# Performance work log

Hardware: AMD Instinct MI355X
Metric: run time of the kernel (lower is better)

The kernel has to match this reference:

```python
import jax, jax.numpy as jnp
import numpy as np

N_NODES = 100000
N_FEAT = 128
HID = 8
HEADS1 = 8
OUT2 = 32
NEG_SLOPE = 0.2


def gat_conv(x, W, a_src, a_dst, b, src, dst, n_nodes, concat):
    # x: [N, Fin], W: [Fin, H*C], a_src/a_dst: [H, C], b: [H*C] or [C]
    H, C = a_src.shape
    h = (x @ W).reshape(n_nodes, H, C)                      # [N, H, C]
    e_src = jnp.sum(h * a_src, axis=-1)                     # [N, H]
    e_dst = jnp.sum(h * a_dst, axis=-1)                     # [N, H]
    e = jax.nn.leaky_relu(e_src[src] + e_dst[dst], NEG_SLOPE)  # [E, H]
    m = jax.ops.segment_max(e, dst, num_segments=n_nodes)   # [N, H] (self-loops => no empty segment)
    ex = jnp.exp(e - m[dst])                                # [E, H]
    denom = jax.ops.segment_sum(ex, dst, num_segments=n_nodes)
    alpha = ex / denom[dst]                                 # [E, H]
    out = jax.ops.segment_sum(alpha[:, :, None] * h[src], dst, num_segments=n_nodes)  # [N, H, C]
    out = out.reshape(n_nodes, H * C) if concat else out.mean(axis=1)
    return out + b


def setup_inputs() -> dict:
    key = jax.random.key(0)
    ks = jax.random.split(key, 12)
    x = jax.random.normal(ks[0], (N_NODES, N_FEAT), dtype=jnp.float32)
    edge_index = jax.random.randint(ks[1], (2, 3200000), 0, N_NODES, dtype=jnp.int64)
    s1 = 1.0 / np.sqrt(N_FEAT)
    s2 = 1.0 / np.sqrt(HID * HEADS1)
    return {
        "x": x,
        "edge_index": edge_index,
        "W1": jax.random.normal(ks[2], (N_FEAT, HEADS1 * HID), dtype=jnp.float32) * s1,
        "a_src1": jax.random.normal(ks[3], (HEADS1, HID), dtype=jnp.float32) * s2,
        "a_dst1": jax.random.normal(ks[4], (HEADS1, HID), dtype=jnp.float32) * s2,
        "b1": jnp.zeros((HEADS1 * HID,), dtype=jnp.float32),
        "W2": jax.random.normal(ks[5], (HEADS1 * HID, OUT2), dtype=jnp.float32) * s2,
        "a_src2": jax.random.normal(ks[6], (1, OUT2), dtype=jnp.float32) * (1.0 / np.sqrt(OUT2)),
        "a_dst2": jax.random.normal(ks[7], (1, OUT2), dtype=jnp.float32) * (1.0 / np.sqrt(OUT2)),
        "b2": jnp.zeros((OUT2,), dtype=jnp.float32),
        "Wr": jax.random.normal(ks[8], (OUT2, 1), dtype=jnp.float32) * (1.0 / np.sqrt(OUT2)),
        "br": jnp.zeros((1,), dtype=jnp.float32),
    }


def reference(x, edge_index, W1, a_src1, a_dst1, b1, W2, a_src2, a_dst2, b2, Wr, br):
    n = x.shape[0]
    # PyG GATConv default add_self_loops=True
    loops = jnp.arange(n, dtype=edge_index.dtype)
    src = jnp.concatenate([edge_index[0], loops])
    dst = jnp.concatenate([edge_index[1], loops])
    h = gat_conv(x, W1, a_src1, a_dst1, b1, src, dst, n, concat=True)   # [N, 64]
    h = jax.nn.elu(h)
    h = gat_conv(h, W2, a_src2, a_dst2, b2, src, dst, n, concat=False)  # [N, 32]
    pooled = jnp.sum(h, axis=0, keepdims=True)                          # SumAggregation -> [1, 32]
    return pooled @ Wr + br                                             # [1, 1]
```

## Files before the change

### kernel.cpp

```cpp
#include <hip/hip_runtime.h>
#include <math.h>

#define NEG_SLOPE 0.2f
#define FIN 128
#define H1 8
#define F1 64
#define F2 32

#define SHIFT 6
#define BW 64
#define CAP 4096
#define NBMAX 2048

typedef unsigned short ushort_t;
typedef unsigned int uint_t;

static __device__ __forceinline__ ushort_t f2bf(float f) {
    uint_t u = __float_as_uint(f);
    u = (u + 0x7FFFu + ((u >> 16) & 1u)) >> 16;
    return (ushort_t)u;
}
static __device__ __forceinline__ float bf2f(ushort_t h) {
    return __uint_as_float(((uint_t)h) << 16);
}
static __device__ __forceinline__ uint_t packAB(float e) {
    return (uint_t)f2bf(__expf(e)) | ((uint_t)f2bf(__expf(NEG_SLOPE * e)) << 16);
}

__global__ void gemm1_kernel(const float* __restrict__ x, const float* __restrict__ W1,
                             const float* __restrict__ a_src, const float* __restrict__ a_dst,
                             ushort_t* __restrict__ h1, uint_t* __restrict__ sp,
                             float* __restrict__ ed, int N) {
    __shared__ float xs[16][FIN];
    int tid = threadIdx.x;
    int n0 = blockIdx.x * 16;
    for (int i = tid; i < 16 * FIN; i += 256) {
        int nn = n0 + (i >> 7);
        xs[i >> 7][i & 127] = (nn < N) ? x[(size_t)nn * FIN + (i & 127)] : 0.f;
    }
    __syncthreads();
    int wv = tid >> 6, j = tid & 63;
    int nb = wv << 2;
    float a0 = 0.f, a1 = 0.f, a2 = 0.f, a3 = 0.f;
#pragma unroll 2
    for (int k = 0; k < FIN; k += 4) {
        float w0 = W1[(k + 0) * F1 + j];
        float w1 = W1[(k + 1) * F1 + j];
        float w2 = W1[(k + 2) * F1 + j];
        float w3 = W1[(k + 3) * F1 + j];
        float4 x0 = *(const float4*)&xs[nb + 0][k];
        float4 x1 = *(const float4*)&xs[nb + 1][k];
        float4 x2 = *(const float4*)&xs[nb + 2][k];
        float4 x3 = *(const float4*)&xs[nb + 3][k];
        a0 = fmaf(x0.x, w0, fmaf(x0.y, w1, fmaf(x0.z, w2, fmaf(x0.w, w3, a0))));
        a1 = fmaf(x1.x, w0, fmaf(x1.y, w1, fmaf(x1.z, w2, fmaf(x1.w, w3, a1))));
        a2 = fmaf(x2.x, w0, fmaf(x2.y, w1, fmaf(x2.z, w2, fmaf(x2.w, w3, a2))));
        a3 = fmaf(x3.x, w0, fmaf(x3.y, w1, fmaf(x3.z, w2, fmaf(x3.w, w3, a3))));
    }
    float as = a_src[j], ad = a_dst[j];
    float av[4] = {a0, a1, a2, a3};
#pragma unroll
    for (int t = 0; t < 4; ++t) {
        int n = n0 + nb + t;
        if (n >= N) break;
        h1[(size_t)n * F1 + j] = f2bf(av[t]);
        float vs = av[t] * as;
        float vd = av[t] * ad;
#pragma unroll
        for (int off = 4; off >= 1; off >>= 1) {
            vs += __shfl_down(vs, off, 8);
            vd += __shfl_down(vd, off, 8);
        }
        if ((j & 7) == 0) {
            sp[n * H1 + (j >> 3)] = packAB(vs);
            ed[n * H1 + (j >> 3)] = vd;
        }
    }
}

__global__ void zerob_kernel(int* __restrict__ bcnt, int NB, float* __restrict__ pooled) {
    int t = blockIdx.x * blockDim.x + threadIdx.x;
    int stride = gridDim.x * blockDim.x;
    for (int i = t; i < NB; i += stride) bcnt[i] = 0;
    if (t == 0) pooled[0] = 0.f;
}

__global__ void bhist_kernel(const int* __restrict__ ei, int E, int N,
                             int* __restrict__ bcnt, int NB) {
    __shared__ int h[NBMAX];
    int tid = threadIdx.x;
    for (int i = tid; i < NB; i += 256) h[i] = 0;
    __syncthreads();
    int EN = E + N;
    int chunk = (EN + gridDim.x - 1) / gridDim.x;
    int e0 = blockIdx.x * chunk;
    int e1 = e0 + chunk; if (e1 > EN) e1 = EN;
    for (int t = e0 + tid; t < e1; t += 256) {
        int d = (t < E) ? ei[E + t] : (t - E);
        atomicAdd(&h[d >> SHIFT], 1);
    }
    __syncthreads();
    for (int i = tid; i < NB; i += 256)
        if (h[i]) atomicAdd(&bcnt[i], h[i]);
}

__global__ void bscan_kernel(const int* __restrict__ bcnt, int NB,
                             int* __restrict__ boff, int* __restrict__ bcur) {
    int lane = threadIdx.x;
    int chunk = (NB + 63) >> 6;
    int lo = lane * chunk;
    int hi = lo + chunk; if (hi > NB) hi = NB;
    int sum = 0;
    for (int i = lo; i < hi; ++i) sum += bcnt[i];
    int e = sum;
#pragma unroll
    for (int o = 1; o < 64; o <<= 1) {
        int v = __shfl_up(e, o, 64);
        if (lane >= o) e += v;
    }
    e -= sum;
    int run = e;
    for (int i = lo; i < hi; ++i) {
        int c = bcnt[i];
        boff[i] = run;
        bcur[i] = run;
        run += c;
    }
}

__global__ void bscat_kernel(const int* __restrict__ ei, int E, int N,
                             int* __restrict__ bcur, uint_t* __restrict__ pk, int NB) {
    __shared__ int lh[NBMAX];
    __shared__ int lc[NBMAX];
    int tid = threadIdx.x;
    for (int i = tid; i < NB; i += 256) lh[i] = 0;
    __syncthreads();
    int EN = E + N;
    int chunk = (EN + gridDim.x - 1) / gridDim.x;
    int e0 = blockIdx.x * chunk;
    int e1 = e0 + chunk; if (e1 > EN) e1 = EN;
    for (int t = e0 + tid; t < e1; t += 256) {
        int d = (t < E) ? ei[E + t] : (t - E);
        atomicAdd(&lh[d >> SHIFT], 1);
    }
    __syncthreads();
    for (int i = tid; i < NB; i += 256) {
        int c = lh[i];
        lc[i] = c ? atomicAdd(&bcur[i], c) : 0;
    }
    __syncthreads();
    for (int t = e0 + tid; t < e1; t += 256) {
        int s, d;
        if (t < E) { s = ei[t]; d = ei[E + t]; } else { s = d = t - E; }
        int pos = atomicAdd(&lc[d >> SHIFT], 1);
        pk[pos] = ((uint_t)s << SHIFT) | (uint_t)(d & (BW - 1));
    }
}

__global__ void edge1_gather(const int* __restrict__ bcnt, const int* __restrict__ boff,
                             const uint_t* __restrict__ pk,
                             const uint_t* __restrict__ sp, const float* __restrict__ ed,
                             const ushort_t* __restrict__ h1, float* __restrict__ o1, int N) {
    int b = blockIdx.x;
    int d0 = b << SHIFT;
    int cnt = bcnt[b];
    int gbase = boff[b];
    int tid = threadIdx.x;
    int wv = tid >> 6;
    int L = tid & 63;
    int q = L >> 4;
    int c4 = (L & 15) << 2;
    int hL = (L & 15) >> 1;
    __shared__ int ldeg[BW];
    __shared__ int loff[BW];
    __shared__ int lcur[BW];
    __shared__ int lsrc[CAP];
    if (cnt <= CAP) {
        if (tid < BW) ldeg[tid] = 0;
        __syncthreads();
        for (int k = tid; k < cnt; k += 256) atomicAdd(&ldeg[pk[gbase + k] & (BW - 1)], 1);
        __syncthreads();
        if (tid < 64) {
            int v = ldeg[tid];
            int e = v;
#pragma unroll
            for (int o = 1; o < 64; o <<= 1) {
                int u = __shfl_up(e, o, 64);
                if (tid >= o) e += u;
            }
            e -= v;
            loff[tid] = e;
            lcur[tid] = e;
        }
        __syncthreads();
        for (int k = tid; k < cnt; k += 256) {
            uint_t v = pk[gbase + k];
            int pos = atomicAdd(&lcur[v & (BW - 1)], 1);
            lsrc[pos] = (int)(v >> SHIFT);
        }
        __syncthreads();
        for (int ld = wv * 16; ld < wv * 16 + 16; ++ld) {
            int d = d0 + ld;
            if (d >= N) break;
            int st = loff[ld], en = st + ldeg[ld];
            float edv = ed[d * H1 + hL];
            float Ad = __expf(edv), Bd = __expf(NEG_SLOPE * edv);
            float ax = 0.f, ay = 0.f, az = 0.f, aw = 0.f, wsum = 0.f;
            for (int k = st; k < en; k += 8) {
                int i0 = k + q, i1 = k + 4 + q;
                bool ok0 = i0 < en, ok1 = i1 < en;
                int s0 = lsrc[ok0 ? i0 : st];
                int s1 = lsrc[ok1 ? i1 : st];
                uint_t u0 = sp[(uint_t)s0 * H1 + hL];
                uint_t u1 = sp[(uint_t)s1 * H1 + hL];
                uint2 hv0 = *(const uint2*)(h1 + ((uint_t)s0 << 6) + c4);
                uint2 hv1 = *(const uint2*)(h1 + ((uint_t)s1 << 6) + c4);
                float w0 = ok0 ? fmaxf(__uint_as_float(u0 << 16) * Ad,
                                       __uint_as_float(u0 & 0xffff0000u) * Bd) : 0.f;
                float w1 = ok1 ? fmaxf(__uint_as_float(u1 << 16) * Ad,
                                       __uint_as_float(u1 & 0xffff0000u) * Bd) : 0.f;
                ax = fmaf(w0, __uint_as_float(hv0.x << 16), ax);
                ay = fmaf(w0, __uint_as_float(hv0.x & 0xffff0000u), ay);
                az = fmaf(w0, __uint_as_float(hv0.y << 16), az);
                aw = fmaf(w0, __uint_as_float(hv0.y & 0xffff0000u), aw);
                ax = fmaf(w1, __uint_as_float(hv1.x << 16), ax);
                ay = fmaf(w1, __uint_as_float(hv1.x & 0xffff0000u), ay);
                az = fmaf(w1, __uint_as_float(hv1.y << 16), az);
                aw = fmaf(w1, __uint_as_float(hv1.y & 0xffff0000u), aw);
                wsum += w0 + w1;
            }
            ax += __shfl_xor(ax, 16, 64); ax += __shfl_xor(ax, 32, 64);
            ay += __shfl_xor(ay, 16, 64); ay += __shfl_xor(ay, 32, 64);
            az += __shfl_xor(az, 16, 64); az += __shfl_xor(az, 32, 64);
            aw += __shfl_xor(aw, 16, 64); aw += __shfl_xor(aw, 32, 64);
            wsum += __shfl_xor(wsum, 16, 64); wsum += __shfl_xor(wsum, 32, 64);
            if (q == 0) {
                float inv = 1.f / wsum;
                float4 r; r.x = ax * inv; r.y = ay * inv; r.z = az * inv; r.w = aw * inv;
                *(float4*)(o1 + (size_t)d * F1 + c4) = r;
            }
        }
    } else {
        for (int ld = wv * 16; ld < wv * 16 + 16; ++ld) {
            int d = d0 + ld;
            if (d >= N) break;
            float edv = ed[d * H1 + hL];
            float Ad = __expf(edv), Bd = __expf(NEG_SLOPE * edv);
            float ax = 0.f, ay = 0.f, az = 0.f, aw = 0.f, wsum = 0.f;
            for (int k0 = 0; k0 < cnt; k0 += 4) {
                int idx = k0 + q;
                bool ok = idx < cnt;
                uint_t v = pk[gbase + (ok ? idx : 0)];
                int s = (int)(v >> SHIFT);
                bool m = ok && ((int)(v & (BW - 1)) == ld);
                uint_t u = sp[(uint_t)s * H1 + hL];
                float w = m ? fmaxf(__uint_as_float(u << 16) * Ad,
                                    __uint_as_float(u & 0xffff0000u) * Bd) : 0.f;
                uint2 hv = *(const uint2*)(h1 + ((uint_t)s << 6) + c4);
                ax = fmaf(w, __uint_as_float(hv.x << 16), ax);
                ay = fmaf(w, __uint_as_float(hv.x & 0xffff0000u), ay);
                az = fmaf(w, __uint_as_float(hv.y << 16), az);
                aw = fmaf(w, __uint_as_float(hv.y & 0xffff0000u), aw);
                wsum += w;
            }
            ax += __shfl_xor(ax, 16, 64); ax += __shfl_xor(ax, 32, 64);
            ay += __shfl_xor(ay, 16, 64); ay += __shfl_xor(ay, 32, 64);
            az += __shfl_xor(az, 16, 64); az += __shfl_xor(az, 32, 64);
            aw += __shfl_xor(aw, 16, 64); aw += __shfl_xor(aw, 32, 64);
            wsum += __shfl_xor(wsum, 16, 64); wsum += __shfl_xor(wsum, 32, 64);
            if (q == 0) {
                float inv = 1.f / wsum;
                float4 r; r.x = ax * inv; r.y = ay * inv; r.z = az * inv; r.w = aw * inv;
                *(float4*)(o1 + (size_t)d * F1 + c4) = r;
            }
        }
    }
}

__global__ void gemm2_kernel(const float* __restrict__ o1, const float* __restrict__ b1,
                             const float* __restrict__ W2,
                             const float* __restrict__ a_src2, const float* __restrict__ a_dst2,
                             ushort_t* __restrict__ h2, uint_t* __restrict__ sp2,
                             float* __restrict__ ed2, int N) {
    int half = threadIdx.x >> 5;
    int n = blockIdx.x * 8 + half;
    int j = threadIdx.x & 31;
    __shared__ float a1s[8][F1];
    if (n < N) {
#pragma unroll
        for (int r = 0; r < 2; ++r) {
            int k = r * 32 + j;
            float v = o1[(size_t)n * F1 + k] + b1[k];
            a1s[half][k] = v > 0.f ? v : expm1f(v);
        }
    }
    __syncthreads();
    if (n >= N) return;
    float acc = 0.f;
#pragma unroll
    for (int k = 0; k < F1; ++k) acc = fmaf(a1s[half][k], W2[k * F2 + j], acc);
    h2[(size_t)n * F2 + j] = f2bf(acc);
    float vs = acc * a_src2[j];
    float vd = acc * a_dst2[j];
#pragma unroll
    for (int off = 16; off >= 1; off >>= 1) {
        vs += __shfl_down(vs, off, 32);
        vd += __shfl_down(vd, off, 32);
    }
    if (j == 0) {
        sp2[n] = packAB(vs);
        ed2[n] = vd;
    }
}

__global__ void edge2_gather(const int* __restrict__ bcnt, const int* __restrict__ boff,
                             const uint_t* __restrict__ pk,
                             const uint_t* __restrict__ sp2, const float* __restrict__ ed2,
                             const ushort_t* __restrict__ h2,
                             const float* __restrict__ b2, const float* __restrict__ Wr,
                             float* __restrict__ pooled, int N) {
    int b = blockIdx.x;
    int d0 = b << SHIFT;
    int cnt = bcnt[b];
    int gbase = boff[b];
    int tid = threadIdx.x;
    int hw = tid >> 5;
    int j = tid & 31;
    __shared__ int ldeg[BW];
    __shared__ int loff[BW];
    __shared__ int lcur[BW];
    __shared__ int lsrc[CAP];
    float wr = Wr[j];
    float b2w = b2[j] * wr;
    float part = 0.f;
    if (cnt <= CAP) {
        if (tid < BW) ldeg[tid] = 0;
        __syncthreads();
        for (int k = tid; k < cnt; k += 256) atomicAdd(&ldeg[pk[gbase + k] & (BW - 1)], 1);
        __syncthreads();
        if (tid < 64) {
            int v = ldeg[tid];
            int e = v;
#pragma unroll
            for (int o = 1; o < 64; o <<= 1) {
                int u = __shfl_up(e, o, 64);
                if (tid >= o) e += u;
            }
            e -= v;
            loff[tid] = e;
            lcur[tid] = e;
        }
        __syncthreads();
        for (int k = tid; k < cnt; k += 256) {
            uint_t v = pk[gbase + k];
            int pos = atomicAdd(&lcur[v & (BW - 1)], 1);
            lsrc[pos] = (int)(v >> SHIFT);
        }
        __syncthreads();
        for (int ld = hw * 8; ld < hw * 8 + 8; ++ld) {
            int d = d0 + ld;
            if (d >= N) break;
            int st = loff[ld], dg = ldeg[ld];
            float edv = ed2[d];
            float Ad = __expf(edv), Bd = __expf(NEG_SLOPE * edv);
            float acc = 0.f, wsum = 0.f;
#pragma unroll 4
            for (int k = st; k < st + dg; ++k) {
                int s = lsrc[k];
                uint_t u = sp2[s];
                float w = fmaxf(__uint_as_float(u << 16) * Ad,
                                __uint_as_float(u & 0xffff0000u) * Bd);
                acc = fmaf(w, bf2f(h2[(size_t)s * F2 + j]), acc);
                wsum += w;
            }
            part = fmaf(acc / wsum, wr, part + b2w);
        }
    } else {
        for (int ld = hw * 8; ld < hw * 8 + 8; ++ld) {
            int d = d0 + ld;
            if (d >= N) break;
            float edv = ed2[d];
            float Ad = __expf(edv), Bd = __expf(NEG_SLOPE * edv);
            float acc = 0.f, wsum = 0.f;
            for (int k = 0; k < cnt; ++k) {
                uint_t v = pk[gbase + k];
                if ((int)(v & (BW - 1)) != ld) continue;
                int s = (int)(v >> SHIFT);
                uint_t u = sp2[s];
                float w = fmaxf(__uint_as_float(u << 16) * Ad,
                                __uint_as_float(u & 0xffff0000u) * Bd);
                acc = fmaf(w, bf2f(h2[(size_t)s * F2 + j]), acc);
                wsum += w;
            }
            part = fmaf(acc / wsum, wr, part + b2w);
        }
    }
#pragma unroll
    for (int o = 32; o >= 1; o >>= 1) part += __shfl_down(part, o, 64);
    __shared__ float ls[4];
    int wave = tid >> 6;
    if ((tid & 63) == 0) ls[wave] = part;
    __syncthreads();
    if (tid == 0) atomicAdd(pooled, ls[0] + ls[1] + ls[2] + ls[3]);
}

__global__ void final_kernel(const float* __restrict__ pooled, const float* __restrict__ br,
                             float* __restrict__ out) {
    if (threadIdx.x == 0 && blockIdx.x == 0) out[0] = pooled[0] + br[0];
}

extern "C" void kernel_launch(void* const* d_in, const int* in_sizes, int n_in,
                              void* d_out, int out_size, void* d_ws, size_t ws_size,
                              hipStream_t stream) {
    const float* x    = (const float*)d_in[0];
    const int*   ei   = (const int*)d_in[1];
    const float* W1   = (const float*)d_in[2];
    const float* a_s1 = (const float*)d_in[3];
    const float* a_d1 = (const float*)d_in[4];
    const float* b1   = (const float*)d_in[5];
    const float* W2   = (const float*)d_in[6];
    const float* a_s2 = (const float*)d_in[7];
    const float* a_d2 = (const float*)d_in[8];
    const float* b2   = (const float*)d_in[9];
    const float* Wr   = (const float*)d_in[10];
    const float* br   = (const float*)d_in[11];
    float* out = (float*)d_out;

    int N = in_sizes[0] / FIN;
    int E = in_sizes[1] / 2;
    size_t n = (size_t)N;
    int NB = (N + BW - 1) >> SHIFT;

    char* ws = (char*)d_ws;
    float*    o1   = (float*)ws;
    uint_t*   sp1  = (uint_t*)(ws + n * 256);
    float*    ed1  = (float*)(ws + n * 288);
    ushort_t* h1   = (ushort_t*)(ws + n * 320);
    uint_t*   pk   = (uint_t*)(ws + n * 448);
    char*     tail = ws + n * 448 + (size_t)(E + N) * 4;
    int*      bcnt = (int*)tail;
    int*      boff = (int*)(tail + NBMAX * 4);
    int*      bcur = (int*)(tail + NBMAX * 8);
    float*  pooled = (float*)(tail + NBMAX * 12);
    ushort_t* h2  = h1;
    uint_t*   sp2 = sp1;
    float*    ed2 = ed1;

    zerob_kernel<<<8, 256, 0, stream>>>(bcnt, NB, pooled);
    gemm1_kernel<<<(N + 15) / 16, 256, 0, stream>>>(x, W1, a_s1, a_d1, h1, sp1, ed1, N);
    bhist_kernel<<<256, 256, 0, stream>>>(ei, E, N, bcnt, NB);
    bscan_kernel<<<1, 64, 0, stream>>>(bcnt, NB, boff, bcur);
    bscat_kernel<<<256, 256, 0, stream>>>(ei, E, N, bcur, pk, NB);
    edge1_gather<<<NB, 256, 0, stream>>>(bcnt, boff, pk, sp1, ed1, h1, o1, N);
    gemm2_kernel<<<(N + 7) / 8, 256, 0, stream>>>(o1, b1, W2, a_s2, a_d2, h2, sp2, ed2, N);
    edge2_gather<<<NB, 256, 0, stream>>>(bcnt, boff, pk, sp2, ed2, h2, b2, Wr, pooled, N);
    final_kernel<<<1, 64, 0, stream>>>(pooled, br, out);
}
```

Baseline: 454.3 us.

## Store per-block bucket histograms to skip recount in scatter pass

The bucket counting kernel now writes each block's per-bucket histogram to global memory, and a new column-wise scan kernel turns those into exact per-block write offsets. The scatter kernel loads its offsets directly instead of re-reading all destination indices, rebuilding the histogram with shared atomics, and reserving ranges with global atomics. This removes one full pass over the destination array plus the contention on shared and global atomics. It costs extra workspace, one more small launch, and a strided serial scan over 256 rows per bucket.

```diff
diff --git a/kernel.cpp b/kernel.cpp
--- a/kernel.cpp
+++ b/kernel.cpp
@@ -11,6 +11,7 @@
 #define BW 64
 #define CAP 4096
 #define NBMAX 2048
+#define NBLK 256
 
 typedef unsigned short ushort_t;
 typedef unsigned int uint_t;
@@ -85,11 +86,11 @@
     if (t == 0) pooled[0] = 0.f;
 }
 
-__global__ void bhist_kernel(const int* __restrict__ ei, int E, int N,
-                             int* __restrict__ bcnt, int NB) {
-    __shared__ int h[NBMAX];
+__global__ void bscat_count(const int* __restrict__ ei, int E, int N,
+                            int* __restrict__ bcnt, int* __restrict__ pcnt, int NB) {
+    __shared__ int lh[NBMAX];
     int tid = threadIdx.x;
-    for (int i = tid; i < NB; i += 256) h[i] = 0;
+    for (int i = tid; i < NB; i += 256) lh[i] = 0;
     __syncthreads();
     int EN = E + N;
     int chunk = (EN + gridDim.x - 1) / gridDim.x;
@@ -97,15 +98,18 @@
     int e1 = e0 + chunk; if (e1 > EN) e1 = EN;
     for (int t = e0 + tid; t < e1; t += 256) {
         int d = (t < E) ? ei[E + t] : (t - E);
-        atomicAdd(&h[d >> SHIFT], 1);
-    }
-    __syncthreads();
-    for (int i = tid; i < NB; i += 256)
-        if (h[i]) atomicAdd(&bcnt[i], h[i]);
-}
-
-__global__ void bscan_kernel(const int* __restrict__ bcnt, int NB,
-                             int* __restrict__ boff, int* __restrict__ bcur) {
+        atomicAdd(&lh[d >> SHIFT], 1);
+    }
+    __syncthreads();
+    int* row = pcnt + (size_t)blockIdx.x * NB;
+    for (int i = tid; i < NB; i += 256) {
+        int c = lh[i];
+        row[i] = c;
+        if (c) atomicAdd(&bcnt[i], c);
+    }
+}
+
+__global__ void bscan_kernel(const int* __restrict__ bcnt, int NB, int* __restrict__ boff) {
     int lane = threadIdx.x;
     int chunk = (NB + 63) >> 6;
     int lo = lane * chunk;
@@ -121,34 +125,33 @@
     e -= sum;
     int run = e;
     for (int i = lo; i < hi; ++i) {
-        int c = bcnt[i];
         boff[i] = run;
-        bcur[i] = run;
+        run += bcnt[i];
+    }
+}
+
+__global__ void bscan2_kernel(const int* __restrict__ boff, int* __restrict__ pcnt, int NB) {
+    int i = blockIdx.x * blockDim.x + threadIdx.x;
+    if (i >= NB) return;
+    int run = boff[i];
+    for (int b = 0; b < NBLK; ++b) {
+        int c = pcnt[(size_t)b * NB + i];
+        pcnt[(size_t)b * NB + i] = run;
         run += c;
     }
 }
 
-__global__ void bscat_kernel(const int* __restrict__ ei, int E, int N,
-                             int* __restrict__ bcur, uint_t* __restrict__ pk, int NB) {
-    __shared__ int lh[NBMAX];
+__global__ void bscat_scatter(const int* __restrict__ ei, int E, int N,
+                              const int* __restrict__ pcnt, uint_t* __restrict__ pk, int NB) {
     __shared__ int lc[NBMAX];
     int tid = threadIdx.x;
-    for (int i = tid; i < NB; i += 256) lh[i] = 0;
+    const int* row = pcnt + (size_t)blockIdx.x * NB;
+    for (int i = tid; i < NB; i += 256) lc[i] = row[i];
     __syncthreads();
     int EN = E + N;
     int chunk = (EN + gridDim.x - 1) / gridDim.x;
     int e0 = blockIdx.x * chunk;
     int e1 = e0 + chunk; if (e1 > EN) e1 = EN;
-    for (int t = e0 + tid; t < e1; t += 256) {
-        int d = (t < E) ? ei[E + t] : (t - E);
-        atomicAdd(&lh[d >> SHIFT], 1);
-    }
-    __syncthreads();
-    for (int i = tid; i < NB; i += 256) {
-        int c = lh[i];
-        lc[i] = c ? atomicAdd(&bcur[i], c) : 0;
-    }
-    __syncthreads();
     for (int t = e0 + tid; t < e1; t += 256) {
         int s, d;
         if (t < E) { s = ei[t]; d = ei[E + t]; } else { s = d = t - E; }
@@ -440,17 +443,18 @@
     char*     tail = ws + n * 448 + (size_t)(E + N) * 4;
     int*      bcnt = (int*)tail;
     int*      boff = (int*)(tail + NBMAX * 4);
-    int*      bcur = (int*)(tail + NBMAX * 8);
-    float*  pooled = (float*)(tail + NBMAX * 12);
+    float*  pooled = (float*)(tail + NBMAX * 8);
+    int*      pcnt = (int*)(tail + NBMAX * 8 + 64);
     ushort_t* h2  = h1;
     uint_t*   sp2 = sp1;
     float*    ed2 = ed1;
 
     zerob_kernel<<<8, 256, 0, stream>>>(bcnt, NB, pooled);
     gemm1_kernel<<<(N + 15) / 16, 256, 0, stream>>>(x, W1, a_s1, a_d1, h1, sp1, ed1, N);
-    bhist_kernel<<<256, 256, 0, stream>>>(ei, E, N, bcnt, NB);
-    bscan_kernel<<<1, 64, 0, stream>>>(bcnt, NB, boff, bcur);
-    bscat_kernel<<<256, 256, 0, stream>>>(ei, E, N, bcur, pk, NB);
+    bscat_count<<<NBLK, 256, 0, stream>>>(ei, E, N, bcnt, pcnt, NB);
+    bscan_kernel<<<1, 64, 0, stream>>>(bcnt, NB, boff);
+    bscan2_kernel<<<(NB + 255) / 256, 256, 0, stream>>>(boff, pcnt, NB);
+    bscat_scatter<<<NBLK, 256, 0, stream>>>(ei, E, N, pcnt, pk, NB);
     edge1_gather<<<NB, 256, 0, stream>>>(bcnt, boff, pk, sp1, ed1, h1, o1, N);
     gemm2_kernel<<<(N + 7) / 8, 256, 0, stream>>>(o1, b1, W2, a_s2, a_d2, h2, sp2, ed2, N);
     edge2_gather<<<NB, 256, 0, stream>>>(bcnt, boff, pk, sp2, ed2, h2, b2, Wr, pooled, N);
```

Measured after the change: 483.7 us. +6.5%, slower.
